# Kernel optimization log

Hardware: AMD Instinct MI355X
Metric: run time of the kernel (lower is better)

The kernel has to match this reference:

```python
import jax, jax.numpy as jnp
import numpy as np
import math

B, S, D, H = 4, 2048, 1024, 8
DH = D // H  # 128
LN_EPS = 1e-5


def setup_inputs() -> dict:
    key = jax.random.key(0)
    ks = jax.random.split(key, 8)
    s = 1.0 / math.sqrt(D)
    return {
        "queries": jax.random.normal(ks[0], (B, S, D), jnp.float32),
        "keys": jax.random.normal(ks[1], (B, S, D), jnp.float32),
        "values": jax.random.normal(ks[2], (B, S, D), jnp.float32),
        "Wq": jax.random.normal(ks[3], (D, D), jnp.float32) * s,
        "Wk": jax.random.normal(ks[4], (D, D), jnp.float32) * s,
        "Wv": jax.random.normal(ks[5], (D, D), jnp.float32) * s,
        "Wr": jax.random.normal(ks[6], (D, D), jnp.float32) * s,
        "ln_gamma": jnp.ones((D,), jnp.float32),
        "ln_beta": jnp.zeros((D,), jnp.float32),
    }


def reference(queries, keys, values, Wq, Wk, Wv, Wr, ln_gamma, ln_beta):
    b, s, d = queries.shape
    dh = d // H
    # torch Linear (bias=False): x @ W.T ; then raw contiguous reshape
    # [B,S,D] -> [B*H, S, D/H] (faithful to the original .view, which splits
    # the sequence into H contiguous chunks, not the channel dim).
    Q = (queries @ Wq.T).reshape(b * H, -1, dh)
    K = (keys @ Wk.T).reshape(b * H, -1, dh)
    V = (values @ Wv.T).reshape(b * H, -1, dh)
    # d_k = Q.shape[2] * 8 (hardcoded 8 in the source)
    scale = 1.0 / math.sqrt(dh * 8)
    scores = jnp.einsum('bqd,bkd->bqk', Q, K) * scale  # [B*H, S, S]
    attn = jax.nn.softmax(scores, axis=-1)
    out = jnp.einsum('bqk,bkd->bqd', attn, V)  # [B*H, S, D/H]
    out = out.reshape(b, -1, dh * H)  # [B, S, D]
    out = out @ Wr.T
    out = out + queries  # residual (dropout_rate=0 -> identity)
    # LayerNorm over last dim, eps=1e-5
    mu = jnp.mean(out, axis=-1, keepdims=True)
    var = jnp.var(out, axis=-1, keepdims=True)
    out = (out - mu) * jax.lax.rsqrt(var + LN_EPS) * ln_gamma + ln_beta
    return out
```

## Files before the change

kernel.cpp:

```cpp
#include <hip/hip_runtime.h>
#include <hip/hip_bf16.h>

constexpr int Tseq = 2048;
constexpr int Gq   = 32;
constexpr int Cd   = 128;

typedef __attribute__((ext_vector_type(4))) float  f32x4;
typedef __attribute__((ext_vector_type(8))) __bf16 bf16x8;
typedef __attribute__((ext_vector_type(4))) __bf16 bf16x4;

#define MFMA16(a, b, c) __builtin_amdgcn_mfma_f32_16x16x32_bf16((a), (b), (c), 0, 0, 0)

__device__ __forceinline__ void glds16(const void* g, void* l) {
    __builtin_amdgcn_global_load_lds(
        (__attribute__((address_space(1))) void*)(const void*)g,
        (__attribute__((address_space(3))) void*)l, 16, 0, 0);
}

__device__ __forceinline__ bf16x4 trread(const void* p) {
    bf16x4 d;
    const unsigned a32 =
        (unsigned)(size_t)(const __attribute__((address_space(3))) __bf16*)p;
    asm volatile("ds_read_b64_tr_b16 %0, %1" : "=v"(d) : "v"(a32));
    return d;
}

__global__ __launch_bounds__(256) void detect_dtype(const unsigned short* __restrict__ q,
                                                    int* __restrict__ flag) {
    __shared__ int cnt;
    if (threadIdx.x == 0) cnt = 0;
    __syncthreads();
    int c = 0;
    for (int i = threadIdx.x; i < 16384; i += 256) {
        const int e = (q[i] >> 7) & 0xFF;
        c += (e == 0xFF || e == 0x00) ? 1 : 0;
    }
    atomicAdd(&cnt, c);
    __syncthreads();
    if (threadIdx.x == 0) flag[0] = (cnt >= 4) ? 1 : 0;
}

__global__ __launch_bounds__(256) void cvt_bf16(const float* __restrict__ in,
                                                __bf16* __restrict__ out,
                                                int n8, const int* __restrict__ flag) {
    const int stride = gridDim.x * 256;
    if (flag[0]) {
        for (int i = blockIdx.x * 256 + threadIdx.x; i < n8; i += stride) {
            const f32x4 a0 = *(const f32x4*)(in + (size_t)i * 8);
            const f32x4 a1 = *(const f32x4*)(in + (size_t)i * 8 + 4);
            bf16x8 pk;
#pragma unroll
            for (int j = 0; j < 4; ++j) { pk[j] = (__bf16)a0[j]; pk[4 + j] = (__bf16)a1[j]; }
            *(bf16x8*)(out + (size_t)i * 8) = pk;
        }
    } else {
        const f32x4* src = (const f32x4*)in;
        for (int i = blockIdx.x * 256 + threadIdx.x; i < n8; i += stride)
            *(f32x4*)((char*)out + (size_t)i * 16) = src[i];
    }
}

__global__ __launch_bounds__(256) void gemm_bt(const void* __restrict__ Ain,
                                               const void* __restrict__ Win,
                                               __bf16* __restrict__ Cout,
                                               const int* __restrict__ flag,
                                               int amode, int wmode) {
    constexpr int K = 1024, N = 1024;
    __shared__ __bf16 As[128 * 64];
    __shared__ __bf16 Ws[128 * 64];
    const bool af32 = amode && (flag[0] != 0);
    const bool wf32 = wmode && (flag[0] != 0);
    const __bf16* Ab = (const __bf16*)Ain;
    const __bf16* Wb = (const __bf16*)Win;
    const float*  Af = (const float*)Ain;
    const float*  Wf = (const float*)Win;

    const int t = threadIdx.x;
    const int lane = t & 63, wid = t >> 6;
    const int wr = wid >> 1, wc = wid & 1;
    const int hw = blockIdx.y * gridDim.x + blockIdx.x;
    const int logical = (hw & 7) * 64 + (hw >> 3);
    const int m0 = (logical >> 3) * 128, n0 = (logical & 7) * 128;
    const int fr = lane & 15, fg = lane >> 4;

    f32x4 acc[4][4] = {};

    for (int k0 = 0; k0 < K; k0 += 64) {
        if (af32) {
#pragma unroll
            for (int p = 0; p < 4; ++p) {
                const int i = p * 256 + t, row = i >> 3, c8 = i & 7;
                const float* ap = Af + (size_t)(m0 + row) * K + k0 + c8 * 8;
                const f32x4 a0 = *(const f32x4*)ap;
                const f32x4 a1 = *(const f32x4*)(ap + 4);
                bf16x8 pk;
#pragma unroll
                for (int j = 0; j < 4; ++j) { pk[j] = (__bf16)a0[j]; pk[4 + j] = (__bf16)a1[j]; }
                *(bf16x8*)((char*)As + (size_t)i * 16) = pk;
            }
        } else {
#pragma unroll
            for (int p = 0; p < 4; ++p) {
                const int i = p * 256 + t, row = i >> 3, c8 = i & 7;
                glds16(Ab + (size_t)(m0 + row) * K + k0 + c8 * 8,
                       (char*)As + (size_t)(p * 256 + wid * 64) * 16);
            }
        }
        if (wf32) {
#pragma unroll
            for (int p = 0; p < 4; ++p) {
                const int i = p * 256 + t, row = i >> 3, c8 = i & 7;
                const float* wp = Wf + (size_t)(n0 + row) * K + k0 + c8 * 8;
                const f32x4 w0 = *(const f32x4*)wp;
                const f32x4 w1 = *(const f32x4*)(wp + 4);
                bf16x8 pk;
#pragma unroll
                for (int j = 0; j < 4; ++j) { pk[j] = (__bf16)w0[j]; pk[4 + j] = (__bf16)w1[j]; }
                *(bf16x8*)((char*)Ws + (size_t)i * 16) = pk;
            }
        } else {
#pragma unroll
            for (int p = 0; p < 4; ++p) {
                const int i = p * 256 + t, row = i >> 3, c8 = i & 7;
                glds16(Wb + (size_t)(n0 + row) * K + k0 + c8 * 8,
                       (char*)Ws + (size_t)(p * 256 + wid * 64) * 16);
            }
        }
        __syncthreads();
#pragma unroll
        for (int kk = 0; kk < 64; kk += 32) {
            bf16x8 af[4], bfr[4];
#pragma unroll
            for (int mi = 0; mi < 4; ++mi)
                af[mi] = *(const bf16x8*)&As[(wr * 64 + mi * 16 + fr) * 64 + kk + fg * 8];
#pragma unroll
            for (int ni = 0; ni < 4; ++ni)
                bfr[ni] = *(const bf16x8*)&Ws[(wc * 64 + ni * 16 + fr) * 64 + kk + fg * 8];
#pragma unroll
            for (int mi = 0; mi < 4; ++mi)
#pragma unroll
                for (int ni = 0; ni < 4; ++ni)
                    acc[mi][ni] = MFMA16(af[mi], bfr[ni], acc[mi][ni]);
        }
        __syncthreads();
    }
#pragma unroll
    for (int mi = 0; mi < 4; ++mi)
#pragma unroll
        for (int ni = 0; ni < 4; ++ni) {
            const int col = n0 + wc * 64 + ni * 16 + fr;
#pragma unroll
            for (int r = 0; r < 4; ++r) {
                const int row = m0 + wr * 64 + mi * 16 + fg * 4 + r;
                Cout[(size_t)row * N + col] = (__bf16)acc[mi][ni][r];
            }
        }
}

__global__ __launch_bounds__(256) void flash_attn(const __bf16* __restrict__ Qg,
                                                  const __bf16* __restrict__ Kg,
                                                  const __bf16* __restrict__ Vg,
                                                  __bf16* __restrict__ Og) {
    constexpr float SCALE = 0.03125f;
    constexpr float MS    = 2.0f;
    __shared__ __bf16 Ks[2][64 * 128];
    __shared__ __bf16 Vs[2][64 * 128];

    const int t = threadIdx.x;
    const int lane = t & 63, wid = t >> 6;
    const int fr = lane & 15, fg = lane >> 4;

    const int hw = blockIdx.y * gridDim.x + blockIdx.x;
    const int logical = (hw & 7) * 64 + (hw >> 3);
    const int grp = logical >> 4;
    const int qtile = logical & 15;

    const size_t hoff = (size_t)grp * Tseq * Cd;
    const __bf16* Qh = Qg + hoff;
    const __bf16* Kh = Kg + hoff;
    const __bf16* Vh = Vg + hoff;
    const int qBase = qtile * 128 + wid * 32;

    const int kRowLo  = t >> 4;
    const int kSrcCol = ((t & 15) * 8) ^ (((t >> 4) & 7) << 3);
    const int swz8    = (fr & 7) << 3;
    const int vtrLane = fg * 1024 + fr * 8;

    bf16x8 qf[2][4];
#pragma unroll
    for (int u = 0; u < 2; ++u)
#pragma unroll
        for (int c4 = 0; c4 < 4; ++c4)
            qf[u][c4] = *(const bf16x8*)(Qh + (size_t)(qBase + u * 16 + fr) * Cd
                                         + c4 * 32 + fg * 8);

    f32x4 acc[8][2] = {};
    float l_run0 = 0.f, l_run1 = 0.f;

    auto stageKV = [&](int ktn, int b) {
#pragma unroll
        for (int p = 0; p < 4; ++p)
            glds16(Kh + (size_t)(ktn + p * 16 + kRowLo) * Cd + kSrcCol,
                   (char*)Ks[b] + (size_t)(p * 256 + wid * 64) * 16);
#pragma unroll
        for (int p = 0; p < 4; ++p) {
            const int j  = p * 256 + t;
            const int kk = ((j >> 6) << 2) + ((j & 7) >> 1);
            const int c0 = (((j >> 3) & 7) << 4) + ((j & 1) << 3);
            glds16(Vh + (size_t)(ktn + kk) * Cd + c0,
                   (char*)Vs[b] + (size_t)(p * 256 + wid * 64) * 16);
        }
    };

    stageKV(0, 0);
    __syncthreads();

    for (int it = 0; it < Tseq / 64; ++it) {
        const int cur = it & 1;
        const __bf16* Kb_ = Ks[cur];
        const char*   Vb_ = (const char*)Vs[cur] + vtrLane;
        if (it + 1 < Tseq / 64) stageKV((it + 1) * 64, cur ^ 1);

#pragma unroll
        for (int s = 0; s < 64; s += 32) {
            f32x4 sA0 = {}, sA1 = {}, sB0 = {}, sB1 = {};
            __builtin_amdgcn_s_setprio(1);
#pragma unroll
            for (int c4 = 0; c4 < 4; ++c4) {
                const int cidx = (c4 * 32 + fg * 8) ^ swz8;
                const bf16x8 k0 = *(const bf16x8*)&Kb_[(s + fr) * 128 + cidx];
                const bf16x8 k1 = *(const bf16x8*)&Kb_[(s + 16 + fr) * 128 + cidx];
                sA0 = MFMA16(k0, qf[0][c4], sA0);
                sA1 = MFMA16(k1, qf[0][c4], sA1);
                sB0 = MFMA16(k0, qf[1][c4], sB0);
                sB1 = MFMA16(k1, qf[1][c4], sB1);
            }
            __builtin_amdgcn_s_setprio(0);

            bf16x4 vlo[8], vhi[8];
            const int soff = (s >> 2) << 10;
#pragma unroll
            for (int ct = 0; ct < 8; ++ct) {
                vlo[ct] = trread(Vb_ + soff + ct * 128);
                vhi[ct] = trread(Vb_ + soff + ct * 128 + 4096);
            }

            bf16x8 pf0, pf1;
            {
                const float p0 = __expf(sA0[0] * SCALE - MS), p1 = __expf(sA0[1] * SCALE - MS);
                const float p2 = __expf(sA0[2] * SCALE - MS), p3 = __expf(sA0[3] * SCALE - MS);
                const float p4 = __expf(sA1[0] * SCALE - MS), p5 = __expf(sA1[1] * SCALE - MS);
                const float p6 = __expf(sA1[2] * SCALE - MS), p7 = __expf(sA1[3] * SCALE - MS);
                float ps = ((p0 + p1) + (p2 + p3)) + ((p4 + p5) + (p6 + p7));
                ps += __shfl_xor(ps, 16);
                ps += __shfl_xor(ps, 32);
                l_run0 += ps;
                pf0[0] = (__bf16)p0; pf0[1] = (__bf16)p1; pf0[2] = (__bf16)p2; pf0[3] = (__bf16)p3;
                pf0[4] = (__bf16)p4; pf0[5] = (__bf16)p5; pf0[6] = (__bf16)p6; pf0[7] = (__bf16)p7;
            }
            {
                const float p0 = __expf(sB0[0] * SCALE - MS), p1 = __expf(sB0[1] * SCALE - MS);
                const float p2 = __expf(sB0[2] * SCALE - MS), p3 = __expf(sB0[3] * SCALE - MS);
                const float p4 = __expf(sB1[0] * SCALE - MS), p5 = __expf(sB1[1] * SCALE - MS);
                const float p6 = __expf(sB1[2] * SCALE - MS), p7 = __expf(sB1[3] * SCALE - MS);
                float ps = ((p0 + p1) + (p2 + p3)) + ((p4 + p5) + (p6 + p7));
                ps += __shfl_xor(ps, 16);
                ps += __shfl_xor(ps, 32);
                l_run1 += ps;
                pf1[0] = (__bf16)p0; pf1[1] = (__bf16)p1; pf1[2] = (__bf16)p2; pf1[3] = (__bf16)p3;
                pf1[4] = (__bf16)p4; pf1[5] = (__bf16)p5; pf1[6] = (__bf16)p6; pf1[7] = (__bf16)p7;
            }

            asm volatile("s_waitcnt lgkmcnt(0)" ::: "memory");
            __builtin_amdgcn_sched_barrier(0);
            __builtin_amdgcn_s_setprio(1);
#pragma unroll
            for (int ct = 0; ct < 8; ++ct) {
                const bf16x8 vf = __builtin_shufflevector(vlo[ct], vhi[ct],
                                                          0, 1, 2, 3, 4, 5, 6, 7);
                acc[ct][0] = MFMA16(vf, pf0, acc[ct][0]);
                acc[ct][1] = MFMA16(vf, pf1, acc[ct][1]);
            }
            __builtin_amdgcn_s_setprio(0);
        }
        __syncthreads();
    }

    const float inv0 = 1.f / l_run0, inv1 = 1.f / l_run1;
#pragma unroll
    for (int ct = 0; ct < 8; ++ct) {
        bf16x4 o0, o1;
#pragma unroll
        for (int r = 0; r < 4; ++r) {
            o0[r] = (__bf16)(acc[ct][0][r] * inv0);
            o1[r] = (__bf16)(acc[ct][1][r] * inv1);
        }
        *(bf16x4*)(Og + hoff + (size_t)(qBase + fr) * Cd + ct * 16 + fg * 4) = o0;
        *(bf16x4*)(Og + hoff + (size_t)(qBase + 16 + fr) * Cd + ct * 16 + fg * 4) = o1;
    }
}

__global__ __launch_bounds__(256) void ln_residual(const __bf16* __restrict__ P,
                                                   const void* __restrict__ Qin,
                                                   const void* __restrict__ gamma,
                                                   const void* __restrict__ beta,
                                                   void* __restrict__ out,
                                                   const int* __restrict__ flag) {
    const bool f32 = (flag[0] != 0);
    const int row = blockIdx.x;
    const int t = threadIdx.x;
    const int lane = t & 63, wid = t >> 6;
    const size_t base = (size_t)row * 1024 + t * 4;

    const bf16x4 pv = *(const bf16x4*)(P + base);
    float x[4], s = 0.f, s2 = 0.f;
    if (f32) {
        const f32x4 qv = *(const f32x4*)((const float*)Qin + base);
#pragma unroll
        for (int j = 0; j < 4; ++j) x[j] = (float)pv[j] + qv[j];
    } else {
        const bf16x4 qv = *(const bf16x4*)((const __bf16*)Qin + base);
#pragma unroll
        for (int j = 0; j < 4; ++j) x[j] = (float)pv[j] + (float)qv[j];
    }
#pragma unroll
    for (int j = 0; j < 4; ++j) { s += x[j]; s2 += x[j] * x[j]; }
#pragma unroll
    for (int off = 32; off >= 1; off >>= 1) {
        s += __shfl_xor(s, off);
        s2 += __shfl_xor(s2, off);
    }
    __shared__ float red[8];
    if (lane == 0) { red[wid] = s; red[4 + wid] = s2; }
    __syncthreads();
    s = red[0] + red[1] + red[2] + red[3];
    s2 = red[4] + red[5] + red[6] + red[7];
    const float mu = s * (1.f / 1024.f);
    const float var = s2 * (1.f / 1024.f) - mu * mu;
    const float rstd = rsqrtf(var + 1e-5f);

    float g4[4], b4[4];
    if (f32) {
        const f32x4 gv = *(const f32x4*)((const float*)gamma + t * 4);
        const f32x4 bv = *(const f32x4*)((const float*)beta + t * 4);
#pragma unroll
        for (int j = 0; j < 4; ++j) { g4[j] = gv[j]; b4[j] = bv[j]; }
    } else {
        const bf16x4 gv = *(const bf16x4*)((const __bf16*)gamma + t * 4);
        const bf16x4 bv = *(const bf16x4*)((const __bf16*)beta + t * 4);
#pragma unroll
        for (int j = 0; j < 4; ++j) { g4[j] = (float)gv[j]; b4[j] = (float)bv[j]; }
    }
    if (f32) {
        f32x4 o;
#pragma unroll
        for (int j = 0; j < 4; ++j) o[j] = (x[j] - mu) * rstd * g4[j] + b4[j];
        *(f32x4*)((float*)out + base) = o;
    } else {
        bf16x4 o;
#pragma unroll
        for (int j = 0; j < 4; ++j) o[j] = (__bf16)((x[j] - mu) * rstd * g4[j] + b4[j]);
        *(bf16x4*)((__bf16*)out + base) = o;
    }
}

extern "C" void kernel_launch(void* const* d_in, const int* in_sizes, int n_in,
                              void* d_out, int out_size, void* d_ws, size_t ws_size,
                              hipStream_t stream) {
    const void* q   = d_in[0];
    const void* k   = d_in[1];
    const void* v   = d_in[2];
    const void* Wq  = d_in[3];
    const void* Wk  = d_in[4];
    const void* Wv  = d_in[5];
    const void* Wr  = d_in[6];
    const void* gam = d_in[7];
    const void* bet = d_in[8];

    constexpr size_t NE = (size_t)8192 * 1024;
    constexpr size_t NW = (size_t)1024 * 1024;
    char* base = (char*)d_ws;
    int*    flag = (int*)base;
    __bf16* Qb = (__bf16*)(base + 256);
    __bf16* Kb = Qb + NE;
    __bf16* Vb = Kb + NE;
    __bf16* AO = Vb + NE;
    __bf16* Pb = Qb;

    const size_t fixed = 256 + 4 * NE * 2;
    const size_t extra = 3 * NE * 2 + 4 * NW * 2;
    const bool conv = ws_size >= fixed + extra + 1024;

    detect_dtype<<<1, 256, 0, stream>>>((const unsigned short*)q, flag);

    const dim3 gg(1024 / 128, 8192 / 128);
    const dim3 ga(Tseq / 128, Gq);
    if (conv) {
        __bf16* qbf = (__bf16*)(base + fixed);
        __bf16* kbf = qbf + NE;
        __bf16* vbf = kbf + NE;
        __bf16* wqb = vbf + NE;
        __bf16* wkb = wqb + NW;
        __bf16* wvb = wkb + NW;
        __bf16* wrb = wvb + NW;
        cvt_bf16<<<4096, 256, 0, stream>>>((const float*)q, qbf, (int)(NE / 8), flag);
        cvt_bf16<<<4096, 256, 0, stream>>>((const float*)k, kbf, (int)(NE / 8), flag);
        cvt_bf16<<<4096, 256, 0, stream>>>((const float*)v, vbf, (int)(NE / 8), flag);
        cvt_bf16<<<512, 256, 0, stream>>>((const float*)Wq, wqb, (int)(NW / 8), flag);
        cvt_bf16<<<512, 256, 0, stream>>>((const float*)Wk, wkb, (int)(NW / 8), flag);
        cvt_bf16<<<512, 256, 0, stream>>>((const float*)Wv, wvb, (int)(NW / 8), flag);
        cvt_bf16<<<512, 256, 0, stream>>>((const float*)Wr, wrb, (int)(NW / 8), flag);
        gemm_bt<<<gg, 256, 0, stream>>>(qbf, wqb, Qb, flag, 0, 0);
        gemm_bt<<<gg, 256, 0, stream>>>(kbf, wkb, Kb, flag, 0, 0);
        gemm_bt<<<gg, 256, 0, stream>>>(vbf, wvb, Vb, flag, 0, 0);
        flash_attn<<<ga, 256, 0, stream>>>(Qb, Kb, Vb, AO);
        gemm_bt<<<gg, 256, 0, stream>>>(AO, wrb, Pb, flag, 0, 0);
    } else {
        gemm_bt<<<gg, 256, 0, stream>>>(q, Wq, Qb, flag, 1, 1);
        gemm_bt<<<gg, 256, 0, stream>>>(k, Wk, Kb, flag, 1, 1);
        gemm_bt<<<gg, 256, 0, stream>>>(v, Wv, Vb, flag, 1, 1);
        flash_attn<<<ga, 256, 0, stream>>>(Qb, Kb, Vb, AO);
        gemm_bt<<<gg, 256, 0, stream>>>(AO, Wr, Pb, flag, 0, 1);
    }
    ln_residual<<<8192, 256, 0, stream>>>(Pb, q, gam, bet, d_out, flag);
}
```

Before: 261.3 us.

## Batch conversions and QKV GEMMs into single launches; widen attention blocks to 512 threads

The seven fp32-to-bf16 conversion launches become one 2D-grid kernel, and the three projection GEMMs become one z-indexed launch that shares a flag-free bf16 GEMM core. This is meant to cut launch gaps and tail idle time between small kernels. Flash attention now runs 512 threads per block over 256 query rows, so each staged K/V tile is shared by twice as many query rows and fewer loads are issued per thread. The cost is fewer attention blocks (256) for the GPU's compute units, and each block must keep its double-buffered K/V in LDS for longer.

```diff
diff --git a/kernel.cpp b/kernel.cpp
--- a/kernel.cpp
+++ b/kernel.cpp
@@ -40,9 +40,21 @@
     if (threadIdx.x == 0) flag[0] = (cnt >= 4) ? 1 : 0;
 }
 
-__global__ __launch_bounds__(256) void cvt_bf16(const float* __restrict__ in,
-                                                __bf16* __restrict__ out,
-                                                int n8, const int* __restrict__ flag) {
+__global__ __launch_bounds__(256) void cvt_all(
+    const float* __restrict__ i0, const float* __restrict__ i1,
+    const float* __restrict__ i2, const float* __restrict__ i3,
+    const float* __restrict__ i4, const float* __restrict__ i5,
+    const float* __restrict__ i6,
+    __bf16* __restrict__ o0, __bf16* __restrict__ o1, __bf16* __restrict__ o2,
+    __bf16* __restrict__ o3, __bf16* __restrict__ o4, __bf16* __restrict__ o5,
+    __bf16* __restrict__ o6,
+    int nBig, int nSmall, const int* __restrict__ flag) {
+    const int y = blockIdx.y;
+    const float* in = y == 0 ? i0 : y == 1 ? i1 : y == 2 ? i2 : y == 3 ? i3
+                    : y == 4 ? i4 : y == 5 ? i5 : i6;
+    __bf16* out = y == 0 ? o0 : y == 1 ? o1 : y == 2 ? o2 : y == 3 ? o3
+                : y == 4 ? o4 : y == 5 ? o5 : o6;
+    const int n8 = (y < 3) ? nBig : nSmall;
     const int stride = gridDim.x * 256;
     if (flag[0]) {
         for (int i = blockIdx.x * 256 + threadIdx.x; i < n8; i += stride) {
@@ -58,6 +70,84 @@
         for (int i = blockIdx.x * 256 + threadIdx.x; i < n8; i += stride)
             *(f32x4*)((char*)out + (size_t)i * 16) = src[i];
     }
+}
+
+__device__ __forceinline__ void gemm_core(const __bf16* __restrict__ Ab,
+                                          const __bf16* __restrict__ Wb,
+                                          __bf16* __restrict__ Cout) {
+    constexpr int K = 1024, N = 1024;
+    __shared__ __bf16 As[128 * 64];
+    __shared__ __bf16 Ws[128 * 64];
+    const int t = threadIdx.x;
+    const int lane = t & 63, wid = t >> 6;
+    const int wr = wid >> 1, wc = wid & 1;
+    const int hw = blockIdx.y * gridDim.x + blockIdx.x;
+    const int logical = (hw & 7) * 64 + (hw >> 3);
+    const int m0 = (logical >> 3) * 128, n0 = (logical & 7) * 128;
+    const int fr = lane & 15, fg = lane >> 4;
+
+    f32x4 acc[4][4] = {};
+
+    for (int k0 = 0; k0 < K; k0 += 64) {
+#pragma unroll
+        for (int p = 0; p < 4; ++p) {
+            const int i = p * 256 + t, row = i >> 3, c8 = i & 7;
+            glds16(Ab + (size_t)(m0 + row) * K + k0 + c8 * 8,
+                   (char*)As + (size_t)(p * 256 + wid * 64) * 16);
+        }
+#pragma unroll
+        for (int p = 0; p < 4; ++p) {
+            const int i = p * 256 + t, row = i >> 3, c8 = i & 7;
+            glds16(Wb + (size_t)(n0 + row) * K + k0 + c8 * 8,
+                   (char*)Ws + (size_t)(p * 256 + wid * 64) * 16);
+        }
+        __syncthreads();
+#pragma unroll
+        for (int kk = 0; kk < 64; kk += 32) {
+            bf16x8 af[4], bfr[4];
+#pragma unroll
+            for (int mi = 0; mi < 4; ++mi)
+                af[mi] = *(const bf16x8*)&As[(wr * 64 + mi * 16 + fr) * 64 + kk + fg * 8];
+#pragma unroll
+            for (int ni = 0; ni < 4; ++ni)
+                bfr[ni] = *(const bf16x8*)&Ws[(wc * 64 + ni * 16 + fr) * 64 + kk + fg * 8];
+#pragma unroll
+            for (int mi = 0; mi < 4; ++mi)
+#pragma unroll
+                for (int ni = 0; ni < 4; ++ni)
+                    acc[mi][ni] = MFMA16(af[mi], bfr[ni], acc[mi][ni]);
+        }
+        __syncthreads();
+    }
+#pragma unroll
+    for (int mi = 0; mi < 4; ++mi)
+#pragma unroll
+        for (int ni = 0; ni < 4; ++ni) {
+            const int col = n0 + wc * 64 + ni * 16 + fr;
+#pragma unroll
+            for (int r = 0; r < 4; ++r) {
+                const int row = m0 + wr * 64 + mi * 16 + fg * 4 + r;
+                Cout[(size_t)row * N + col] = (__bf16)acc[mi][ni][r];
+            }
+        }
+}
+
+__global__ __launch_bounds__(256) void gemm_qkv(
+    const __bf16* __restrict__ A0, const __bf16* __restrict__ A1,
+    const __bf16* __restrict__ A2,
+    const __bf16* __restrict__ W0, const __bf16* __restrict__ W1,
+    const __bf16* __restrict__ W2,
+    __bf16* __restrict__ C0, __bf16* __restrict__ C1, __bf16* __restrict__ C2) {
+    const int z = blockIdx.z;
+    gemm_core(z == 0 ? A0 : z == 1 ? A1 : A2,
+              z == 0 ? W0 : z == 1 ? W1 : W2,
+              z == 0 ? C0 : z == 1 ? C1 : C2);
+}
+
+__global__ __launch_bounds__(256) void gemm_one(const __bf16* __restrict__ A,
+                                                const __bf16* __restrict__ W,
+                                                __bf16* __restrict__ C) {
+    gemm_core(A, W, C);
 }
 
 __global__ __launch_bounds__(256) void gemm_bt(const void* __restrict__ Ain,
@@ -74,7 +164,6 @@
     const __bf16* Wb = (const __bf16*)Win;
     const float*  Af = (const float*)Ain;
     const float*  Wf = (const float*)Win;
-
     const int t = threadIdx.x;
     const int lane = t & 63, wid = t >> 6;
     const int wr = wid >> 1, wc = wid & 1;
@@ -82,9 +171,7 @@
     const int logical = (hw & 7) * 64 + (hw >> 3);
     const int m0 = (logical >> 3) * 128, n0 = (logical & 7) * 128;
     const int fr = lane & 15, fg = lane >> 4;
-
     f32x4 acc[4][4] = {};
-
     for (int k0 = 0; k0 < K; k0 += 64) {
         if (af32) {
 #pragma unroll
@@ -157,7 +244,7 @@
         }
 }
 
-__global__ __launch_bounds__(256) void flash_attn(const __bf16* __restrict__ Qg,
+__global__ __launch_bounds__(512) void flash_attn(const __bf16* __restrict__ Qg,
                                                   const __bf16* __restrict__ Kg,
                                                   const __bf16* __restrict__ Vg,
                                                   __bf16* __restrict__ Og) {
@@ -171,15 +258,15 @@
     const int fr = lane & 15, fg = lane >> 4;
 
     const int hw = blockIdx.y * gridDim.x + blockIdx.x;
-    const int logical = (hw & 7) * 64 + (hw >> 3);
-    const int grp = logical >> 4;
-    const int qtile = logical & 15;
+    const int logical = (hw & 7) * 32 + (hw >> 3);
+    const int grp = logical >> 3;
+    const int qtile = logical & 7;
 
     const size_t hoff = (size_t)grp * Tseq * Cd;
     const __bf16* Qh = Qg + hoff;
     const __bf16* Kh = Kg + hoff;
     const __bf16* Vh = Vg + hoff;
-    const int qBase = qtile * 128 + wid * 32;
+    const int qBase = qtile * 256 + wid * 32;
 
     const int kRowLo  = t >> 4;
     const int kSrcCol = ((t & 15) * 8) ^ (((t >> 4) & 7) << 3);
@@ -199,16 +286,16 @@
 
     auto stageKV = [&](int ktn, int b) {
 #pragma unroll
-        for (int p = 0; p < 4; ++p)
-            glds16(Kh + (size_t)(ktn + p * 16 + kRowLo) * Cd + kSrcCol,
-                   (char*)Ks[b] + (size_t)(p * 256 + wid * 64) * 16);
-#pragma unroll
-        for (int p = 0; p < 4; ++p) {
-            const int j  = p * 256 + t;
+        for (int p = 0; p < 2; ++p)
+            glds16(Kh + (size_t)(ktn + p * 32 + kRowLo) * Cd + kSrcCol,
+                   (char*)Ks[b] + (size_t)(p * 512 + wid * 64) * 16);
+#pragma unroll
+        for (int p = 0; p < 2; ++p) {
+            const int j  = p * 512 + t;
             const int kk = ((j >> 6) << 2) + ((j & 7) >> 1);
             const int c0 = (((j >> 3) & 7) << 4) + ((j & 1) << 3);
             glds16(Vh + (size_t)(ktn + kk) * Cd + c0,
-                   (char*)Vs[b] + (size_t)(p * 256 + wid * 64) * 16);
+                   (char*)Vs[b] + (size_t)(p * 512 + wid * 64) * 16);
         }
     };
 
@@ -394,7 +481,7 @@
     detect_dtype<<<1, 256, 0, stream>>>((const unsigned short*)q, flag);
 
     const dim3 gg(1024 / 128, 8192 / 128);
-    const dim3 ga(Tseq / 128, Gq);
+    const dim3 ga(Tseq / 256, Gq);
     if (conv) {
         __bf16* qbf = (__bf16*)(base + fixed);
         __bf16* kbf = qbf + NE;
@@ -403,23 +490,21 @@
         __bf16* wkb = wqb + NW;
         __bf16* wvb = wkb + NW;
         __bf16* wrb = wvb + NW;
-        cvt_bf16<<<4096, 256, 0, stream>>>((const float*)q, qbf, (int)(NE / 8), flag);
-        cvt_bf16<<<4096, 256, 0, stream>>>((const float*)k, kbf, (int)(NE / 8), flag);
-        cvt_bf16<<<4096, 256, 0, stream>>>((const float*)v, vbf, (int)(NE / 8), flag);
-        cvt_bf16<<<512, 256, 0, stream>>>((const float*)Wq, wqb, (int)(NW / 8), flag);
-        cvt_bf16<<<512, 256, 0, stream>>>((const float*)Wk, wkb, (int)(NW / 8), flag);
-        cvt_bf16<<<512, 256, 0, stream>>>((const float*)Wv, wvb, (int)(NW / 8), flag);
-        cvt_bf16<<<512, 256, 0, stream>>>((const float*)Wr, wrb, (int)(NW / 8), flag);
-        gemm_bt<<<gg, 256, 0, stream>>>(qbf, wqb, Qb, flag, 0, 0);
-        gemm_bt<<<gg, 256, 0, stream>>>(kbf, wkb, Kb, flag, 0, 0);
-        gemm_bt<<<gg, 256, 0, stream>>>(vbf, wvb, Vb, flag, 0, 0);
-        flash_attn<<<ga, 256, 0, stream>>>(Qb, Kb, Vb, AO);
-        gemm_bt<<<gg, 256, 0, stream>>>(AO, wrb, Pb, flag, 0, 0);
+        cvt_all<<<dim3(2048, 7), 256, 0, stream>>>(
+            (const float*)q, (const float*)k, (const float*)v,
+            (const float*)Wq, (const float*)Wk, (const float*)Wv, (const float*)Wr,
+            qbf, kbf, vbf, wqb, wkb, wvb, wrb,
+            (int)(NE / 8), (int)(NW / 8), flag);
+        gemm_qkv<<<dim3(8, 64, 3), 256, 0, stream>>>(qbf, kbf, vbf,
+                                                     wqb, wkb, wvb,
+                                                     Qb, Kb, Vb);
+        flash_attn<<<ga, 512, 0, stream>>>(Qb, Kb, Vb, AO);
+        gemm_one<<<gg, 256, 0, stream>>>(AO, wrb, Pb);
     } else {
         gemm_bt<<<gg, 256, 0, stream>>>(q, Wq, Qb, flag, 1, 1);
         gemm_bt<<<gg, 256, 0, stream>>>(k, Wk, Kb, flag, 1, 1);
         gemm_bt<<<gg, 256, 0, stream>>>(v, Wv, Vb, flag, 1, 1);
-        flash_attn<<<ga, 256, 0, stream>>>(Qb, Kb, Vb, AO);
+        flash_attn<<<ga, 512, 0, stream>>>(Qb, Kb, Vb, AO);
         gemm_bt<<<gg, 256, 0, stream>>>(AO, Wr, Pb, flag, 0, 1);
     }
     ln_residual<<<8192, 256, 0, stream>>>(Pb, q, gam, bet, d_out, flag);
```

New measurement: 250.0 us. -4.3%, faster.
